# Optimization experiments

Measured on AMD Instinct MI355X. Metric: run time of the kernel, lower is better.

Reference implementation:

```python
import jax, jax.numpy as jnp
import numpy as np

B, T, V, E, DH, H, M, W = 64, 50, 32000, 64, 128, 8, 256, 50


def setup_inputs() -> dict:
    key = jax.random.key(0)
    ks = jax.random.split(key, 18)
    sc = 0.02
    return {
        "x": jax.random.randint(ks[0], (B, T), 0, V),
        "tok_emb": jax.random.normal(ks[1], (V, E)) * sc,
        "pos_emb": jax.random.normal(ks[2], (W, E)) * sc,
        "Wq": jax.random.normal(ks[3], (H, E, DH)) * sc,
        "bq": jnp.zeros((H, DH)),
        "Wk": jax.random.normal(ks[4], (H, E, DH)) * sc,
        "bk": jnp.zeros((H, DH)),
        "Wv": jax.random.normal(ks[5], (H, E, DH)) * sc,
        "bv": jnp.zeros((H, DH)),
        "Wo": jax.random.normal(ks[6], (H * DH, E)) * sc,
        "bo": jnp.zeros((E,)),
        "W1": jax.random.normal(ks[7], (E, M)) * sc,
        "b1": jnp.zeros((M,)),
        "W2": jax.random.normal(ks[8], (M, E)) * sc,
        "b2": jnp.zeros((E,)),
        "Wf": jax.random.normal(ks[9], (E, V)) * sc,
        "bf": jnp.zeros((V,)),
    }


def reference(x, tok_emb, pos_emb, Wq, bq, Wk, bk, Wv, bv, Wo, bo, W1, b1, W2, b2, Wf, bf):
    b, t = x.shape
    h = tok_emb[x] + pos_emb[:t]  # [B,T,E]
    # batched per-head QKV projections (original loops over 8 heads)
    Q = jnp.einsum("bte,hed->bhtd", h, Wq) + bq[None, :, None, :]
    K = jnp.einsum("bte,hed->bhtd", h, Wk) + bk[None, :, None, :]
    Vv = jnp.einsum("bte,hed->bhtd", h, Wv) + bv[None, :, None, :]
    scores = jnp.einsum("bhtd,bhsd->bhts", Q, K) / (DH ** 0.5)
    # faithful to original: masked_fill(tril(scores) == 0, -inf)
    scores = jnp.where(jnp.tril(scores) == 0, -jnp.inf, scores)
    attn = jax.nn.softmax(scores, axis=-1)
    o = jnp.einsum("bhts,bhsd->bhtd", attn, Vv)
    o = o.transpose(0, 2, 1, 3).reshape(b, t, H * DH)  # concat heads
    a = o @ Wo + bo
    # NOTE: no residual connections in the original module
    m = jax.nn.gelu(a @ W1 + b1, approximate=False)
    y = m @ W2 + b2
    logits = y @ Wf + bf  # [B,T,V]
    return logits
```

## Files before the change

### kernel.cpp

```cpp
#include <hip/hip_runtime.h>
#include <math.h>

#define T_ 50
#define R_ 3200

using u16 = unsigned short;
typedef __attribute__((ext_vector_type(8))) __bf16 bf16x8;
typedef __attribute__((ext_vector_type(4))) float f32x4;

__device__ __forceinline__ float bf2f(u16 u) {
  union { unsigned int i; float f; } x; x.i = ((unsigned int)u) << 16; return x.f;
}
__device__ __forceinline__ u16 f2bf(float f) {
  union { float f; unsigned int i; } x; x.f = f;
  unsigned int r = x.i + 0x7FFFu + ((x.i >> 16) & 1u);
  return (u16)(r >> 16);
}
__device__ __forceinline__ void split2(float v, u16& hi, u16& lo) {
  hi = f2bf(v);
  lo = f2bf(v - bf2f(hi));
}
__device__ __forceinline__ float gelu_f(float v) {
  return 0.5f * v * (1.0f + erff(v * 0.70710678118654752f));
}

__global__ __launch_bounds__(256) void k_prep(
    const int* __restrict__ x, const float* __restrict__ tok, const float* __restrict__ pos,
    const float* __restrict__ Wq, const float* __restrict__ Wk, const float* __restrict__ Wv,
    const float* __restrict__ bq, const float* __restrict__ bk, const float* __restrict__ bv,
    const float* __restrict__ Wo, const float* __restrict__ W1, const float* __restrict__ W2,
    const float* __restrict__ Wf,
    u16* __restrict__ hH, u16* __restrict__ hL,
    u16* __restrict__ WqkvTh, u16* __restrict__ WqkvTl, float* __restrict__ bqkv,
    u16* __restrict__ WoTh, u16* __restrict__ WoTl,
    u16* __restrict__ W1Th, u16* __restrict__ W1Tl,
    u16* __restrict__ W2Th, u16* __restrict__ W2Tl,
    u16* __restrict__ WfTh, u16* __restrict__ WfTl) {
  __shared__ __align__(16) float tile[64][68];
  int bid = blockIdx.x;
  if (bid < 800) {
    int i = bid * 256 + threadIdx.x;
    int row = i >> 6, e = i & 63;
    int t = row % T_;
    int v = x[row];
    split2(tok[(long)v * 64 + e] + pos[t * 64 + e], hH[i], hL[i]);
    return;
  }
  if (bid < 1964) {
    int i = (bid - 800) * 256 + threadIdx.x;
    const int S0 = 196608, S1 = 3072, S2 = 65536, S3 = 16384;
    if (i < S0) {
      int n = i >> 6, e = i & 63;
      int p = n >> 10, rem = n & 1023;
      int hh_ = rem >> 7, d = rem & 127;
      const float* W = (p == 0) ? Wq : ((p == 1) ? Wk : Wv);
      split2(W[hh_ * 8192 + e * 128 + d], WqkvTh[i], WqkvTl[i]);
      return;
    }
    i -= S0;
    if (i < S1) { int p = i >> 10, rem = i & 1023;
      const float* bb = (p == 0) ? bq : ((p == 1) ? bk : bv);
      bqkv[i] = bb[rem]; return; }
    i -= S1;
    if (i < S2) { int n = i >> 10, k = i & 1023;
      split2(Wo[k * 64 + n], WoTh[i], WoTl[i]); return; }
    i -= S2;
    if (i < S3) { int n = i >> 6, k = i & 63;
      split2(W1[k * 256 + n], W1Th[i], W1Tl[i]); return; }
    i -= S3;
    { int n = i >> 8, k = i & 255;
      split2(W2[k * 64 + n], W2Th[i], W2Tl[i]); }
    return;
  }
  int n0 = (bid - 1964) * 64;
  for (int c = threadIdx.x; c < 1024; c += 256) {
    int k = c >> 4, ch = (c & 15) * 4;
    *(float4*)&tile[k][ch] = *(const float4*)&Wf[(long)k * 32000 + n0 + ch];
  }
  __syncthreads();
  for (int c = threadIdx.x; c < 1024; c += 256) {
    int n = c >> 4, ch = (c & 15) * 4;
    u16 th[4], tl[4];
#pragma unroll
    for (int j = 0; j < 4; ++j) split2(tile[ch + j][n], th[j], tl[j]);
    *(ushort4*)&WfTh[(long)(n0 + n) * 64 + ch] = *(ushort4*)th;
    *(ushort4*)&WfTl[(long)(n0 + n) * 64 + ch] = *(ushort4*)tl;
  }
}

__global__ __launch_bounds__(256) void k_attn(const float* __restrict__ QKV,
                                              u16* __restrict__ Oh,
                                              u16* __restrict__ Ol) {
  __shared__ __align__(16) float Kl[64 * 128];
  __shared__ __align__(16) float Vt[128 * 64];
  __shared__ __align__(16) float Qw[4][512];
  __shared__ __align__(16) float Pw[4][256];
  const int bh = blockIdx.x, b = bh >> 3, hd = bh & 7;
  const int tid = threadIdx.x, lane = tid & 63, wave = tid >> 6;
  const float* base = QKV + (long)b * T_ * 3072 + hd * 128;
  for (int c = tid; c < 64 * 32; c += 256) {
    int s = c >> 5, c4 = c & 31;
    float4 kv = make_float4(0.f, 0.f, 0.f, 0.f), vv = kv;
    if (s < T_) {
      const float* rowp = base + (long)s * 3072;
      kv = *(const float4*)(rowp + 1024 + c4 * 4);
      vv = *(const float4*)(rowp + 2048 + c4 * 4);
    }
    *(float4*)&Kl[s * 128 + ((c4 ^ (s & 31)) << 2)] = kv;
    int d0 = c4 * 4, s4 = s >> 2, sm = s & 3;
    Vt[(d0 + 0) * 64 + ((s4 ^ ((d0 + 0) & 15)) << 2) + sm] = vv.x;
    Vt[(d0 + 1) * 64 + ((s4 ^ ((d0 + 1) & 15)) << 2) + sm] = vv.y;
    Vt[(d0 + 2) * 64 + ((s4 ^ ((d0 + 2) & 15)) << 2) + sm] = vv.z;
    Vt[(d0 + 3) * 64 + ((s4 ^ ((d0 + 3) & 15)) << 2) + sm] = vv.w;
  }
  __syncthreads();
  const float scale = 0.0883883476483184406f;
  for (int g = wave; g < 13; g += 4) {
    const int r0 = g * 4;
#pragma unroll
    for (int it = 0; it < 2; ++it) {
      int cc = lane + it * 64;
      int j = cc >> 5, c4q = cc & 31;
      int rq = r0 + j;
      if (rq < T_)
        *(float4*)&Qw[wave][j * 128 + c4q * 4] =
            *(const float4*)&base[(long)rq * 3072 + c4q * 4];
    }
    asm volatile("s_waitcnt lgkmcnt(0)" ::: "memory");
    float p0 = 0.f, p1 = 0.f, p2 = 0.f, p3 = 0.f;
#pragma unroll 8
    for (int c4 = 0; c4 < 32; ++c4) {
      float4 kv = *(const float4*)&Kl[lane * 128 + ((c4 ^ (lane & 31)) << 2)];
      float4 q0 = *(const float4*)&Qw[wave][c4 * 4];
      float4 q1 = *(const float4*)&Qw[wave][128 + c4 * 4];
      float4 q2 = *(const float4*)&Qw[wave][256 + c4 * 4];
      float4 q3 = *(const float4*)&Qw[wave][384 + c4 * 4];
      p0 = fmaf(q0.x, kv.x, p0); p0 = fmaf(q0.y, kv.y, p0);
      p0 = fmaf(q0.z, kv.z, p0); p0 = fmaf(q0.w, kv.w, p0);
      p1 = fmaf(q1.x, kv.x, p1); p1 = fmaf(q1.y, kv.y, p1);
      p1 = fmaf(q1.z, kv.z, p1); p1 = fmaf(q1.w, kv.w, p1);
      p2 = fmaf(q2.x, kv.x, p2); p2 = fmaf(q2.y, kv.y, p2);
      p2 = fmaf(q2.z, kv.z, p2); p2 = fmaf(q2.w, kv.w, p2);
      p3 = fmaf(q3.x, kv.x, p3); p3 = fmaf(q3.y, kv.y, p3);
      p3 = fmaf(q3.z, kv.z, p3); p3 = fmaf(q3.w, kv.w, p3);
    }
    float ps[4] = {p0, p1, p2, p3};
#pragma unroll
    for (int j = 0; j < 4; ++j) {
      int rq = r0 + j;
      float sc = (rq < T_ && lane <= rq) ? ps[j] * scale : -INFINITY;
      float mx = sc;
      mx = fmaxf(mx, __shfl_xor(mx, 32)); mx = fmaxf(mx, __shfl_xor(mx, 16));
      mx = fmaxf(mx, __shfl_xor(mx, 8));  mx = fmaxf(mx, __shfl_xor(mx, 4));
      mx = fmaxf(mx, __shfl_xor(mx, 2));  mx = fmaxf(mx, __shfl_xor(mx, 1));
      float e = expf(sc - mx);
      float sum = e;
      sum += __shfl_xor(sum, 32); sum += __shfl_xor(sum, 16); sum += __shfl_xor(sum, 8);
      sum += __shfl_xor(sum, 4);  sum += __shfl_xor(sum, 2);  sum += __shfl_xor(sum, 1);
      Pw[wave][j * 64 + lane] = e / sum;
    }
    asm volatile("s_waitcnt lgkmcnt(0)" ::: "memory");
    float oa[4] = {0.f, 0.f, 0.f, 0.f};
    float ob[4] = {0.f, 0.f, 0.f, 0.f};
    for (int s4 = 0; s4 <= g; ++s4) {
      int vc = (s4 ^ (lane & 15)) << 2;
      float4 va = *(const float4*)&Vt[lane * 64 + vc];
      float4 vb = *(const float4*)&Vt[(64 + lane) * 64 + vc];
#pragma unroll
      for (int j = 0; j < 4; ++j) {
        float4 pb = *(const float4*)&Pw[wave][j * 64 + s4 * 4];
        oa[j] = fmaf(pb.x, va.x, oa[j]); oa[j] = fmaf(pb.y, va.y, oa[j]);
        oa[j] = fmaf(pb.z, va.z, oa[j]); oa[j] = fmaf(pb.w, va.w, oa[j]);
        ob[j] = fmaf(pb.x, vb.x, ob[j]); ob[j] = fmaf(pb.y, vb.y, ob[j]);
        ob[j] = fmaf(pb.z, vb.z, ob[j]); ob[j] = fmaf(pb.w, vb.w, ob[j]);
      }
    }
#pragma unroll
    for (int j = 0; j < 4; ++j) {
      int rq = r0 + j;
      if (rq < T_) {
        long orow = ((long)b * T_ + rq) * 1024 + hd * 128;
        u16 hi, lo;
        split2(oa[j], hi, lo); Oh[orow + lane] = hi;      Ol[orow + lane] = lo;
        split2(ob[j], hi, lo); Oh[orow + 64 + lane] = hi; Ol[orow + 64 + lane] = lo;
      }
    }
  }
}

template <int BN, int BK, int ACT, int OSPLIT, int SWZ>
__global__ __launch_bounds__(256) void k_gemm(
    const u16* __restrict__ Ah, const u16* __restrict__ Al,
    const u16* __restrict__ Bth, const u16* __restrict__ Btl,
    const float* __restrict__ bias,
    float* __restrict__ C, u16* __restrict__ Ch, u16* __restrict__ Cl,
    int ldc, int K, int gm) {
  constexpr int BM = 64;
  constexpr int TN = BN / 16;
  constexpr int BKW = BK / 8;
  __shared__ __align__(16) u16 Bh[BN][BK + 8];
  __shared__ __align__(16) u16 Bl[BN][BK + 8];
  int id = blockIdx.x;
  if constexpr (SWZ) {
    int nbk = gridDim.x;
    int q = nbk >> 3, r = nbk & 7;
    int xcd = id & 7, idx = id >> 3;
    id = (xcd < r ? xcd * (q + 1) : r * (q + 1) + (xcd - r) * q) + idx;
  }
  const int m0 = (id % gm) * BM, n0 = (id / gm) * BN;
  const int tid = threadIdx.x, lane = tid & 63, wave = tid >> 6;
  const int ln = lane & 15, quad = lane >> 4;
  const int mrow = m0 + wave * 16 + ln;
  const long arow = (long)mrow * K;
  f32x4 acc[TN];
#pragma unroll
  for (int tn = 0; tn < TN; ++tn)
#pragma unroll
    for (int i = 0; i < 4; ++i) acc[tn][i] = 0.f;

  for (int kk = 0; kk < K; kk += BK) {
#pragma unroll
    for (int c0 = 0; c0 < BN * BKW; c0 += 256) {
      int c = c0 + tid;
      int rr = c / BKW, c8 = (c % BKW) * 8;
      *(uint4*)&Bh[rr][c8] = *(const uint4*)&Bth[(long)(n0 + rr) * K + kk + c8];
      *(uint4*)&Bl[rr][c8] = *(const uint4*)&Btl[(long)(n0 + rr) * K + kk + c8];
    }
    __syncthreads();
#pragma unroll
    for (int ks = 0; ks < BK / 32; ++ks) {
      bf16x8 a_h = *(const bf16x8*)&Ah[arow + kk + ks * 32 + quad * 8];
      bf16x8 a_l = *(const bf16x8*)&Al[arow + kk + ks * 32 + quad * 8];
#pragma unroll
      for (int tn = 0; tn < TN; ++tn) {
        bf16x8 b_h = *(const bf16x8*)&Bh[tn * 16 + ln][ks * 32 + quad * 8];
        bf16x8 b_l = *(const bf16x8*)&Bl[tn * 16 + ln][ks * 32 + quad * 8];
        acc[tn] = __builtin_amdgcn_mfma_f32_16x16x32_bf16(b_h, a_h, acc[tn], 0, 0, 0);
        acc[tn] = __builtin_amdgcn_mfma_f32_16x16x32_bf16(b_h, a_l, acc[tn], 0, 0, 0);
        acc[tn] = __builtin_amdgcn_mfma_f32_16x16x32_bf16(b_l, a_h, acc[tn], 0, 0, 0);
      }
    }
    __syncthreads();
  }
#pragma unroll
  for (int tn = 0; tn < TN; ++tn) {
    int nc = n0 + tn * 16 + quad * 4;
    float4 bv = *(const float4*)&bias[nc];
    float v0 = acc[tn][0] + bv.x, v1 = acc[tn][1] + bv.y;
    float v2 = acc[tn][2] + bv.z, v3 = acc[tn][3] + bv.w;
    if (ACT) { v0 = gelu_f(v0); v1 = gelu_f(v1); v2 = gelu_f(v2); v3 = gelu_f(v3); }
    long idx2 = (long)mrow * ldc + nc;
    if constexpr (OSPLIT) {
      ushort4 hs, ls;
      split2(v0, hs.x, ls.x); split2(v1, hs.y, ls.y);
      split2(v2, hs.z, ls.z); split2(v3, hs.w, ls.w);
      *(ushort4*)&Ch[idx2] = hs;
      *(ushort4*)&Cl[idx2] = ls;
    } else {
      *(float4*)&C[idx2] = make_float4(v0, v1, v2, v3);
    }
  }
}

extern "C" void kernel_launch(void* const* d_in, const int* in_sizes, int n_in,
                              void* d_out, int out_size, void* d_ws, size_t ws_size,
                              hipStream_t stream) {
  const int*   x   = (const int*)d_in[0];
  const float* tok = (const float*)d_in[1];
  const float* pos = (const float*)d_in[2];
  const float* Wq  = (const float*)d_in[3];
  const float* bq  = (const float*)d_in[4];
  const float* Wk  = (const float*)d_in[5];
  const float* bk  = (const float*)d_in[6];
  const float* Wv  = (const float*)d_in[7];
  const float* bv  = (const float*)d_in[8];
  const float* Wo  = (const float*)d_in[9];
  const float* bo  = (const float*)d_in[10];
  const float* W1  = (const float*)d_in[11];
  const float* b1  = (const float*)d_in[12];
  const float* W2  = (const float*)d_in[13];
  const float* b2  = (const float*)d_in[14];
  const float* Wf  = (const float*)d_in[15];
  const float* bfv = (const float*)d_in[16];

  char* ws = (char*)d_ws;
  float* QKV    = (float*)(ws + 0);
  u16*   oH     = (u16*)(ws + 39321600);
  u16*   oL     = (u16*)(ws + 45875200);
  u16*   hH     = (u16*)(ws + 52428800);
  u16*   hL     = (u16*)(ws + 52838400);
  u16*   aH     = (u16*)(ws + 53248000);
  u16*   aL     = (u16*)(ws + 53657600);
  u16*   mH     = (u16*)(ws + 54067200);
  u16*   mL     = (u16*)(ws + 55705600);
  u16*   yH     = (u16*)(ws + 57344000);
  u16*   yL     = (u16*)(ws + 57753600);
  u16*   WqkvTh = (u16*)(ws + 58163200);
  u16*   WqkvTl = (u16*)(ws + 58556416);
  float* bqkv   = (float*)(ws + 58949632);
  u16*   WoTh   = (u16*)(ws + 58961920);
  u16*   WoTl   = (u16*)(ws + 59092992);
  u16*   W1Th   = (u16*)(ws + 59224064);
  u16*   W1Tl   = (u16*)(ws + 59256832);
  u16*   W2Th   = (u16*)(ws + 59289600);
  u16*   W2Tl   = (u16*)(ws + 59322368);
  u16*   WfTh   = (u16*)(ws + 59355136);
  u16*   WfTl   = (u16*)(ws + 63451136);
  float* out    = (float*)d_out;

  k_prep<<<dim3(2464), 256, 0, stream>>>(x, tok, pos, Wq, Wk, Wv, bq, bk, bv,
      Wo, W1, W2, Wf, hH, hL, WqkvTh, WqkvTl, bqkv, WoTh, WoTl,
      W1Th, W1Tl, W2Th, W2Tl, WfTh, WfTl);
  k_gemm<128, 64, 0, 0, 0><<<dim3(1200), 256, 0, stream>>>(
      hH, hL, WqkvTh, WqkvTl, bqkv, QKV, nullptr, nullptr, 3072, 64, 50);
  k_attn<<<dim3(512), 256, 0, stream>>>(QKV, oH, oL);
  k_gemm<64, 256, 0, 1, 0><<<dim3(50), 256, 0, stream>>>(
      oH, oL, WoTh, WoTl, bo, nullptr, aH, aL, 64, 1024, 50);
  k_gemm<128, 64, 1, 1, 0><<<dim3(100), 256, 0, stream>>>(
      aH, aL, W1Th, W1Tl, b1, nullptr, mH, mL, 256, 64, 50);
  k_gemm<64, 256, 0, 1, 0><<<dim3(50), 256, 0, stream>>>(
      mH, mL, W2Th, W2Tl, b2, nullptr, yH, yL, 64, 256, 50);
  k_gemm<128, 64, 0, 0, 1><<<dim3(12500), 256, 0, stream>>>(
      yH, yL, WfTh, WfTl, bfv, out, nullptr, nullptr, 32000, 64, 50);
}
```

Measured before the change: 602.7 us.

## Fuse QKV projection into attention and Wo/W1/W2 MLP chain into one kernel

```diff
diff --git a/kernel.cpp b/kernel.cpp
--- a/kernel.cpp
+++ b/kernel.cpp
@@ -88,53 +88,79 @@
   }
 }
 
-__global__ __launch_bounds__(256) void k_attn(const float* __restrict__ QKV,
-                                              u16* __restrict__ Oh,
-                                              u16* __restrict__ Ol) {
+__global__ __launch_bounds__(256) void k_attn(
+    const u16* __restrict__ hH, const u16* __restrict__ hL,
+    const u16* __restrict__ WqkvTh, const u16* __restrict__ WqkvTl,
+    const float* __restrict__ bqkv,
+    u16* __restrict__ Oh, u16* __restrict__ Ol) {
   __shared__ __align__(16) float Kl[64 * 128];
   __shared__ __align__(16) float Vt[128 * 64];
-  __shared__ __align__(16) float Qw[4][512];
+  __shared__ __align__(16) float Qall[64][132];
   __shared__ __align__(16) float Pw[4][256];
   const int bh = blockIdx.x, b = bh >> 3, hd = bh & 7;
   const int tid = threadIdx.x, lane = tid & 63, wave = tid >> 6;
-  const float* base = QKV + (long)b * T_ * 3072 + hd * 128;
-  for (int c = tid; c < 64 * 32; c += 256) {
-    int s = c >> 5, c4 = c & 31;
-    float4 kv = make_float4(0.f, 0.f, 0.f, 0.f), vv = kv;
-    if (s < T_) {
-      const float* rowp = base + (long)s * 3072;
-      kv = *(const float4*)(rowp + 1024 + c4 * 4);
-      vv = *(const float4*)(rowp + 2048 + c4 * 4);
-    }
-    *(float4*)&Kl[s * 128 + ((c4 ^ (s & 31)) << 2)] = kv;
-    int d0 = c4 * 4, s4 = s >> 2, sm = s & 3;
-    Vt[(d0 + 0) * 64 + ((s4 ^ ((d0 + 0) & 15)) << 2) + sm] = vv.x;
-    Vt[(d0 + 1) * 64 + ((s4 ^ ((d0 + 1) & 15)) << 2) + sm] = vv.y;
-    Vt[(d0 + 2) * 64 + ((s4 ^ ((d0 + 2) & 15)) << 2) + sm] = vv.z;
-    Vt[(d0 + 3) * 64 + ((s4 ^ ((d0 + 3) & 15)) << 2) + sm] = vv.w;
+  const int ln = lane & 15, quad = lane >> 4;
+  const int m = wave * 16 + ln;
+  const long arow = ((long)b * T_ + m) * 64;
+  f32x4 acc[24];
+#pragma unroll
+  for (int t = 0; t < 24; ++t)
+#pragma unroll
+    for (int i = 0; i < 4; ++i) acc[t][i] = 0.f;
+#pragma unroll
+  for (int ks = 0; ks < 2; ++ks) {
+    bf16x8 a_h = *(const bf16x8*)&hH[arow + ks * 32 + quad * 8];
+    bf16x8 a_l = *(const bf16x8*)&hL[arow + ks * 32 + quad * 8];
+#pragma unroll
+    for (int t = 0; t < 24; ++t) {
+      const long brow =
+          (long)((t >> 3) * 1024 + hd * 128 + (t & 7) * 16 + ln) * 64 + ks * 32 + quad * 8;
+      bf16x8 b_h = *(const bf16x8*)&WqkvTh[brow];
+      bf16x8 b_l = *(const bf16x8*)&WqkvTl[brow];
+      acc[t] = __builtin_amdgcn_mfma_f32_16x16x32_bf16(b_h, a_h, acc[t], 0, 0, 0);
+      acc[t] = __builtin_amdgcn_mfma_f32_16x16x32_bf16(b_h, a_l, acc[t], 0, 0, 0);
+      acc[t] = __builtin_amdgcn_mfma_f32_16x16x32_bf16(b_l, a_h, acc[t], 0, 0, 0);
+    }
+  }
+#pragma unroll
+  for (int t = 0; t < 8; ++t) {
+    float4 bv = *(const float4*)&bqkv[hd * 128 + t * 16 + quad * 4];
+    *(float4*)&Qall[m][t * 16 + quad * 4] = make_float4(
+        acc[t][0] + bv.x, acc[t][1] + bv.y, acc[t][2] + bv.z, acc[t][3] + bv.w);
+  }
+#pragma unroll
+  for (int t = 0; t < 8; ++t) {
+    float4 bv = *(const float4*)&bqkv[1024 + hd * 128 + t * 16 + quad * 4];
+    int c4 = t * 4 + quad;
+    *(float4*)&Kl[m * 128 + ((c4 ^ (m & 31)) << 2)] = make_float4(
+        acc[8 + t][0] + bv.x, acc[8 + t][1] + bv.y,
+        acc[8 + t][2] + bv.z, acc[8 + t][3] + bv.w);
+  }
+#pragma unroll
+  for (int t = 0; t < 8; ++t) {
+    float4 bv = *(const float4*)&bqkv[2048 + hd * 128 + t * 16 + quad * 4];
+    float v0 = acc[16 + t][0] + bv.x, v1 = acc[16 + t][1] + bv.y;
+    float v2 = acc[16 + t][2] + bv.z, v3 = acc[16 + t][3] + bv.w;
+    if (m >= T_) { v0 = 0.f; v1 = 0.f; v2 = 0.f; v3 = 0.f; }
+    int d0 = t * 16 + quad * 4;
+    int s4 = m >> 2, sm = m & 3;
+    Vt[(d0 + 0) * 64 + ((s4 ^ ((d0 + 0) & 15)) << 2) + sm] = v0;
+    Vt[(d0 + 1) * 64 + ((s4 ^ ((d0 + 1) & 15)) << 2) + sm] = v1;
+    Vt[(d0 + 2) * 64 + ((s4 ^ ((d0 + 2) & 15)) << 2) + sm] = v2;
+    Vt[(d0 + 3) * 64 + ((s4 ^ ((d0 + 3) & 15)) << 2) + sm] = v3;
   }
   __syncthreads();
   const float scale = 0.0883883476483184406f;
   for (int g = wave; g < 13; g += 4) {
     const int r0 = g * 4;
-#pragma unroll
-    for (int it = 0; it < 2; ++it) {
-      int cc = lane + it * 64;
-      int j = cc >> 5, c4q = cc & 31;
-      int rq = r0 + j;
-      if (rq < T_)
-        *(float4*)&Qw[wave][j * 128 + c4q * 4] =
-            *(const float4*)&base[(long)rq * 3072 + c4q * 4];
-    }
-    asm volatile("s_waitcnt lgkmcnt(0)" ::: "memory");
     float p0 = 0.f, p1 = 0.f, p2 = 0.f, p3 = 0.f;
 #pragma unroll 8
     for (int c4 = 0; c4 < 32; ++c4) {
       float4 kv = *(const float4*)&Kl[lane * 128 + ((c4 ^ (lane & 31)) << 2)];
-      float4 q0 = *(const float4*)&Qw[wave][c4 * 4];
-      float4 q1 = *(const float4*)&Qw[wave][128 + c4 * 4];
-      float4 q2 = *(const float4*)&Qw[wave][256 + c4 * 4];
-      float4 q3 = *(const float4*)&Qw[wave][384 + c4 * 4];
+      float4 q0 = *(const float4*)&Qall[r0 + 0][c4 * 4];
+      float4 q1 = *(const float4*)&Qall[r0 + 1][c4 * 4];
+      float4 q2 = *(const float4*)&Qall[r0 + 2][c4 * 4];
+      float4 q3 = *(const float4*)&Qall[r0 + 3][c4 * 4];
       p0 = fmaf(q0.x, kv.x, p0); p0 = fmaf(q0.y, kv.y, p0);
       p0 = fmaf(q0.z, kv.z, p0); p0 = fmaf(q0.w, kv.w, p0);
       p1 = fmaf(q1.x, kv.x, p1); p1 = fmaf(q1.y, kv.y, p1);
@@ -185,6 +211,98 @@
         split2(ob[j], hi, lo); Oh[orow + 64 + lane] = hi; Ol[orow + 64 + lane] = lo;
       }
     }
+  }
+}
+
+__global__ __launch_bounds__(256) void k_mlp(
+    const u16* __restrict__ oH, const u16* __restrict__ oL,
+    const u16* __restrict__ WoTh, const u16* __restrict__ WoTl, const float* __restrict__ bo,
+    const u16* __restrict__ W1Th, const u16* __restrict__ W1Tl, const float* __restrict__ b1,
+    const u16* __restrict__ W2Th, const u16* __restrict__ W2Tl, const float* __restrict__ b2,
+    u16* __restrict__ yH, u16* __restrict__ yL) {
+  __shared__ __align__(16) u16 aLh[16][72], aLl[16][72];
+  __shared__ __align__(16) u16 mLh[16][272], mLl[16][272];
+  const int tid = threadIdx.x, lane = tid & 63, wave = tid >> 6;
+  const int ln = lane & 15, quad = lane >> 4;
+  const long r = (long)blockIdx.x * 16 + ln;
+  f32x4 acc1;
+#pragma unroll
+  for (int i = 0; i < 4; ++i) acc1[i] = 0.f;
+#pragma unroll 4
+  for (int k0 = 0; k0 < 1024; k0 += 32) {
+    bf16x8 a_h = *(const bf16x8*)&oH[r * 1024 + k0 + quad * 8];
+    bf16x8 a_l = *(const bf16x8*)&oL[r * 1024 + k0 + quad * 8];
+    const int brow = (wave * 16 + ln) * 1024 + k0 + quad * 8;
+    bf16x8 b_h = *(const bf16x8*)&WoTh[brow];
+    bf16x8 b_l = *(const bf16x8*)&WoTl[brow];
+    acc1 = __builtin_amdgcn_mfma_f32_16x16x32_bf16(b_h, a_h, acc1, 0, 0, 0);
+    acc1 = __builtin_amdgcn_mfma_f32_16x16x32_bf16(b_h, a_l, acc1, 0, 0, 0);
+    acc1 = __builtin_amdgcn_mfma_f32_16x16x32_bf16(b_l, a_h, acc1, 0, 0, 0);
+  }
+  {
+    int nc = wave * 16 + quad * 4;
+    float4 bv = *(const float4*)&bo[nc];
+    ushort4 hs, ls;
+    split2(acc1[0] + bv.x, hs.x, ls.x); split2(acc1[1] + bv.y, hs.y, ls.y);
+    split2(acc1[2] + bv.z, hs.z, ls.z); split2(acc1[3] + bv.w, hs.w, ls.w);
+    *(ushort4*)&aLh[ln][nc] = hs;
+    *(ushort4*)&aLl[ln][nc] = ls;
+  }
+  __syncthreads();
+  f32x4 acc2[4];
+#pragma unroll
+  for (int t = 0; t < 4; ++t)
+#pragma unroll
+    for (int i = 0; i < 4; ++i) acc2[t][i] = 0.f;
+#pragma unroll
+  for (int k0 = 0; k0 < 64; k0 += 32) {
+    bf16x8 a_h = *(const bf16x8*)&aLh[ln][k0 + quad * 8];
+    bf16x8 a_l = *(const bf16x8*)&aLl[ln][k0 + quad * 8];
+#pragma unroll
+    for (int t = 0; t < 4; ++t) {
+      const int brow = (wave * 64 + t * 16 + ln) * 64 + k0 + quad * 8;
+      bf16x8 b_h = *(const bf16x8*)&W1Th[brow];
+      bf16x8 b_l = *(const bf16x8*)&W1Tl[brow];
+      acc2[t] = __builtin_amdgcn_mfma_f32_16x16x32_bf16(b_h, a_h, acc2[t], 0, 0, 0);
+      acc2[t] = __builtin_amdgcn_mfma_f32_16x16x32_bf16(b_h, a_l, acc2[t], 0, 0, 0);
+      acc2[t] = __builtin_amdgcn_mfma_f32_16x16x32_bf16(b_l, a_h, acc2[t], 0, 0, 0);
+    }
+  }
+#pragma unroll
+  for (int t = 0; t < 4; ++t) {
+    int nc = wave * 64 + t * 16 + quad * 4;
+    float4 bv = *(const float4*)&b1[nc];
+    ushort4 hs, ls;
+    split2(gelu_f(acc2[t][0] + bv.x), hs.x, ls.x);
+    split2(gelu_f(acc2[t][1] + bv.y), hs.y, ls.y);
+    split2(gelu_f(acc2[t][2] + bv.z), hs.z, ls.z);
+    split2(gelu_f(acc2[t][3] + bv.w), hs.w, ls.w);
+    *(ushort4*)&mLh[ln][nc] = hs;
+    *(ushort4*)&mLl[ln][nc] = ls;
+  }
+  __syncthreads();
+  f32x4 acc3;
+#pragma unroll
+  for (int i = 0; i < 4; ++i) acc3[i] = 0.f;
+#pragma unroll 2
+  for (int k0 = 0; k0 < 256; k0 += 32) {
+    bf16x8 a_h = *(const bf16x8*)&mLh[ln][k0 + quad * 8];
+    bf16x8 a_l = *(const bf16x8*)&mLl[ln][k0 + quad * 8];
+    const int brow = (wave * 16 + ln) * 256 + k0 + quad * 8;
+    bf16x8 b_h = *(const bf16x8*)&W2Th[brow];
+    bf16x8 b_l = *(const bf16x8*)&W2Tl[brow];
+    acc3 = __builtin_amdgcn_mfma_f32_16x16x32_bf16(b_h, a_h, acc3, 0, 0, 0);
+    acc3 = __builtin_amdgcn_mfma_f32_16x16x32_bf16(b_h, a_l, acc3, 0, 0, 0);
+    acc3 = __builtin_amdgcn_mfma_f32_16x16x32_bf16(b_l, a_h, acc3, 0, 0, 0);
+  }
+  {
+    int nc = wave * 16 + quad * 4;
+    float4 bv = *(const float4*)&b2[nc];
+    ushort4 hs, ls;
+    split2(acc3[0] + bv.x, hs.x, ls.x); split2(acc3[1] + bv.y, hs.y, ls.y);
+    split2(acc3[2] + bv.z, hs.z, ls.z); split2(acc3[3] + bv.w, hs.w, ls.w);
+    *(ushort4*)&yH[r * 64 + nc] = hs;
+    *(ushort4*)&yL[r * 64 + nc] = ls;
   }
 }
 
@@ -284,42 +402,31 @@
   const float* bfv = (const float*)d_in[16];
 
   char* ws = (char*)d_ws;
-  float* QKV    = (float*)(ws + 0);
-  u16*   oH     = (u16*)(ws + 39321600);
-  u16*   oL     = (u16*)(ws + 45875200);
-  u16*   hH     = (u16*)(ws + 52428800);
-  u16*   hL     = (u16*)(ws + 52838400);
-  u16*   aH     = (u16*)(ws + 53248000);
-  u16*   aL     = (u16*)(ws + 53657600);
-  u16*   mH     = (u16*)(ws + 54067200);
-  u16*   mL     = (u16*)(ws + 55705600);
-  u16*   yH     = (u16*)(ws + 57344000);
-  u16*   yL     = (u16*)(ws + 57753600);
-  u16*   WqkvTh = (u16*)(ws + 58163200);
-  u16*   WqkvTl = (u16*)(ws + 58556416);
-  float* bqkv   = (float*)(ws + 58949632);
-  u16*   WoTh   = (u16*)(ws + 58961920);
-  u16*   WoTl   = (u16*)(ws + 59092992);
-  u16*   W1Th   = (u16*)(ws + 59224064);
-  u16*   W1Tl   = (u16*)(ws + 59256832);
-  u16*   W2Th   = (u16*)(ws + 59289600);
-  u16*   W2Tl   = (u16*)(ws + 59322368);
-  u16*   WfTh   = (u16*)(ws + 59355136);
-  u16*   WfTl   = (u16*)(ws + 63451136);
+  u16*   hH     = (u16*)(ws + 0);
+  u16*   hL     = (u16*)(ws + 417792);
+  u16*   oH     = (u16*)(ws + 835584);
+  u16*   oL     = (u16*)(ws + 7389184);
+  u16*   yH     = (u16*)(ws + 13942784);
+  u16*   yL     = (u16*)(ws + 14352384);
+  u16*   WqkvTh = (u16*)(ws + 14761984);
+  u16*   WqkvTl = (u16*)(ws + 15155200);
+  float* bqkv   = (float*)(ws + 15548416);
+  u16*   WoTh   = (u16*)(ws + 15560704);
+  u16*   WoTl   = (u16*)(ws + 15691776);
+  u16*   W1Th   = (u16*)(ws + 15822848);
+  u16*   W1Tl   = (u16*)(ws + 15855616);
+  u16*   W2Th   = (u16*)(ws + 15888384);
+  u16*   W2Tl   = (u16*)(ws + 15921152);
+  u16*   WfTh   = (u16*)(ws + 15953920);
+  u16*   WfTl   = (u16*)(ws + 20049920);
   float* out    = (float*)d_out;
 
   k_prep<<<dim3(2464), 256, 0, stream>>>(x, tok, pos, Wq, Wk, Wv, bq, bk, bv,
       Wo, W1, W2, Wf, hH, hL, WqkvTh, WqkvTl, bqkv, WoTh, WoTl,
       W1Th, W1Tl, W2Th, W2Tl, WfTh, WfTl);
-  k_gemm<128, 64, 0, 0, 0><<<dim3(1200), 256, 0, stream>>>(
-      hH, hL, WqkvTh, WqkvTl, bqkv, QKV, nullptr, nullptr, 3072, 64, 50);
-  k_attn<<<dim3(512), 256, 0, stream>>>(QKV, oH, oL);
-  k_gemm<64, 256, 0, 1, 0><<<dim3(50), 256, 0, stream>>>(
-      oH, oL, WoTh, WoTl, bo, nullptr, aH, aL, 64, 1024, 50);
-  k_gemm<128, 64, 1, 1, 0><<<dim3(100), 256, 0, stream>>>(
-      aH, aL, W1Th, W1Tl, b1, nullptr, mH, mL, 256, 64, 50);
-  k_gemm<64, 256, 0, 1, 0><<<dim3(50), 256, 0, stream>>>(
-      mH, mL, W2Th, W2Tl, b2, nullptr, yH, yL, 64, 256, 50);
+  k_attn<<<dim3(512), 256, 0, stream>>>(hH, hL, WqkvTh, WqkvTl, bqkv, oH, oL);
+  k_mlp<<<dim3(200), 256, 0, stream>>>(oH, oL, WoTh, WoTl, bo,
+      W1Th, W1Tl, b1, W2Th, W2Tl, b2, yH, yL);
   k_gemm<128, 64, 0, 0, 1><<<dim3(12500), 256, 0, stream>>>(
       yH, yL, WfTh, WfTl, bfv, out, nullptr, nullptr, 32000, 64, 50);
 }
```

Result: no change. 600.3 us (-0.4%).
